# Kernel tuning notes

Measured on AMD Instinct MI355X. Metric: run time of the kernel, lower is better.

Reference implementation:

```python
import jax, jax.numpy as jnp
import numpy as np

N_HEADS = 16
SEG_LEN = 512
MSG_LEN = 1536
T_TOTAL = SEG_LEN + MSG_LEN  # 2048


def _build_mask(T):
    # rows < SEG_LEN: attend to all cols < SEG_LEN (full, non-causal block)
    # rows >= SEG_LEN: standard causal (cols <= row)
    rows = jnp.arange(T)[:, None]
    cols = jnp.arange(T)[None, :]
    mask = jnp.where(rows < SEG_LEN, cols < SEG_LEN, cols <= rows)
    return mask  # [T, T] bool


def setup_inputs() -> dict:
    key = jax.random.key(0)
    k1, k2, k3 = jax.random.split(key, 3)
    B, T, E = 4, T_TOTAL, 1024
    x = jax.random.normal(k1, (B, T, E), dtype=jnp.float32)
    W_qkv = jax.random.normal(k2, (E, 3 * E), dtype=jnp.float32) * (1.0 / np.sqrt(E))
    b_qkv = jnp.zeros((3 * E,), dtype=jnp.float32)
    W_proj = jax.random.normal(k3, (E, E), dtype=jnp.float32) * (1.0 / np.sqrt(E))
    b_proj = jnp.zeros((E,), dtype=jnp.float32)
    return {"x": x, "W_qkv": W_qkv, "b_qkv": b_qkv, "W_proj": W_proj, "b_proj": b_proj}


def reference(x, W_qkv, b_qkv, W_proj, b_proj):
    B, T, E = x.shape
    H = N_HEADS
    D = E // H
    qkv = x @ W_qkv + b_qkv  # [B, T, 3E]
    q, k, v = jnp.split(qkv, 3, axis=-1)
    # [B, H, T, D]
    q = q.reshape(B, T, H, D).transpose(0, 2, 1, 3)
    k = k.reshape(B, T, H, D).transpose(0, 2, 1, 3)
    v = v.reshape(B, T, H, D).transpose(0, 2, 1, 3)
    att = jnp.einsum("bhqd,bhkd->bhqk", q, k) * (1.0 / np.sqrt(D))
    mask = _build_mask(T)  # [T, T]
    att = jnp.where(mask[None, None], att, jnp.float32(-jnp.inf))
    att = jax.nn.softmax(att, axis=-1)
    y = jnp.einsum("bhqk,bhkd->bhqd", att, v)
    y = y.transpose(0, 2, 1, 3).reshape(B, T, E)
    return y @ W_proj + b_proj
```

## Files before the change

### kernel.cpp

```cpp
#include <hip/hip_runtime.h>


typedef _Float16 f16;
typedef _Float16 f16x4 __attribute__((ext_vector_type(4)));
typedef _Float16 f16x8 __attribute__((ext_vector_type(8)));
typedef float f32x4 __attribute__((ext_vector_type(4)));

#define MFMA16x32(a, b, c) __builtin_amdgcn_mfma_f32_16x16x32_f16(a, b, c, 0, 0, 0)
#define MFMA16x16(a, b, c) __builtin_amdgcn_mfma_f32_16x16x16f16(a, b, c, 0, 0, 0)

__device__ __forceinline__ void gload_lds16(const void* g, void* l) {
  __builtin_amdgcn_global_load_lds(
      (__attribute__((address_space(1))) void*)g,
      (__attribute__((address_space(3))) void*)l, 16, 0, 0);
}


__global__ void k_cast_f16(const float* __restrict__ x, f16* __restrict__ xh) {
  int i = blockIdx.x * 256 + threadIdx.x;
  float4 v = ((const float4*)x)[i];
  f16x4 o = {(f16)v.x, (f16)v.y, (f16)v.z, (f16)v.w};
  ((f16x4*)xh)[i] = o;
}

__global__ void k_transpose(const float* __restrict__ W, f16* __restrict__ Wt,
                            int Kdim, int Ndim) {
  __shared__ float tile[32][33];
  int n = blockIdx.x * 32 + threadIdx.x;
  int k0 = blockIdx.y * 32;
  for (int j = threadIdx.y; j < 32; j += 8)
    tile[j][threadIdx.x] = W[(size_t)(k0 + j) * Ndim + n];
  __syncthreads();
  int k = k0 + threadIdx.x;
  for (int j = threadIdx.y; j < 32; j += 8)
    Wt[(size_t)(blockIdx.x * 32 + j) * Kdim + k] = (f16)tile[threadIdx.x][j];
}


__global__ __launch_bounds__(256) void k_gemm_qkv(
    const f16* __restrict__ A, const f16* __restrict__ Bt,
    const float* __restrict__ bias,
    f16* __restrict__ Qo, f16* __restrict__ Ko, f16* __restrict__ Vo) {
  constexpr int KD = 1024;
  __shared__ __align__(16) f16 smem[2 * 128 * 64];
  f16* As = smem;
  f16* Bs = smem + 128 * 64;
  const int tid = threadIdx.x;
  const int wave = tid >> 6, lane = tid & 63;
  const int g = lane >> 4, l16 = lane & 15;
  const int m0 = blockIdx.y * 128, n0 = blockIdx.x * 128;
  const int wm = (wave >> 1) * 64, wn = (wave & 1) * 64;
  const int srow = wave * 8 + (lane >> 3);
  const int skc = ((lane & 7) ^ (lane >> 3)) * 8;

  f32x4 acc[4][4] = {};

  for (int k0 = 0; k0 < KD; k0 += 64) {
    __syncthreads();
    for (int it = 0; it < 4; ++it) {
      gload_lds16(A + (size_t)(m0 + it * 32 + srow) * KD + k0 + skc,
                  As + (it * 32 + wave * 8) * 64);
      gload_lds16(Bt + (size_t)(n0 + it * 32 + srow) * KD + k0 + skc,
                  Bs + (it * 32 + wave * 8) * 64);
    }
    __syncthreads();
    for (int kk = 0; kk < 64; kk += 32) {
      const int ks = kk >> 3;
      f16x8 af[4], bf[4];
      for (int mi = 0; mi < 4; ++mi) {
        int R = wm + mi * 16 + l16, sw = R & 7;
        af[mi] = *(const f16x8*)(As + R * 64 + ((ks + g) ^ sw) * 8);
      }
      for (int ni = 0; ni < 4; ++ni) {
        int R = wn + ni * 16 + l16, sw = R & 7;
        bf[ni] = *(const f16x8*)(Bs + R * 64 + ((ks + g) ^ sw) * 8);
      }
      for (int mi = 0; mi < 4; ++mi)
        for (int ni = 0; ni < 4; ++ni)
          acc[mi][ni] = MFMA16x32(af[mi], bf[ni], acc[mi][ni]);
    }
  }

  const int nsub = n0 + wn;
  const int part = nsub >> 10;
  const int h    = (nsub >> 6) & 15;
  const int mg   = m0 + wm;
  const int b    = mg >> 11;
  const int tb   = mg & 2047;
  const size_t bh = (size_t)(b * 16 + h);

  float bv[4];
  for (int ni = 0; ni < 4; ++ni) bv[ni] = bias[nsub + ni * 16 + l16];

  __syncthreads();
  f16* Es = smem + wave * 4096;

  for (int mi = 0; mi < 4; ++mi)
    for (int ni = 0; ni < 4; ++ni)
      for (int r = 0; r < 4; ++r) {
        f16 hv = (f16)(acc[mi][ni][r] + bv[ni]);
        int mrow = mi * 16 + g * 4 + r, ncol = ni * 16 + l16;
        if (part == 2)
          Es[ncol * 64 + (mrow ^ ((ncol & 7) << 3))] = hv;
        else
          Es[mrow * 64 + (ncol ^ ((mrow & 7) << 3))] = hv;
      }

  const int rrow = lane >> 3, rj = lane & 7;
  for (int p = 0; p < 8; ++p) {
    int row = p * 8 + rrow;
    f16x8 vv = *(const f16x8*)(Es + row * 64 + (rj ^ (row & 7)) * 8);
    int rcol = rj * 8;
    if (part == 0)
      *(f16x8*)(Qo + (bh * 2048 + tb + row) * 64 + rcol) = vv;
    else if (part == 1)
      *(f16x8*)(Ko + (bh * 2048 + tb + row) * 64 + rcol) = vv;
    else
      *(f16x8*)(Vo + (bh * 64 + row) * 2048 + tb + rcol) = vv;
  }
}


__global__ __launch_bounds__(512, 4) void k_attn(
    const f16* __restrict__ Q, const f16* __restrict__ Kb,
    const f16* __restrict__ Vt, f16* __restrict__ Y) {
  __shared__ __align__(16) f16 Ks[2][64 * 64];
  __shared__ __align__(16) f16 Vs[2][64 * 64];
  __shared__ __align__(16) f16 Es[8 * 32 * 72];
  __shared__ float rs[8 * 32];

  const int tid = threadIdx.x;
  const int wave = tid >> 6, lane = tid & 63;
  const int wlo = wave & 3;
  const int g = lane >> 4, l16 = lane & 15;
  const int bh = blockIdx.x;
  const int b = bh >> 4, h = bh & 15;
  const int p = (blockIdx.x + blockIdx.y) & 7;
  const int qa = 15 - 2 * p;
  const int qt = (wave >> 2) ? (qa - 1) : qa;
  const int q0 = qt * 128;
  const int ntq = (qt < 4) ? 8 : (qt + 1) * 2;
  const int nta = (qa < 4) ? 8 : (qa + 1) * 2;
  const int srowrel = lane >> 3;
  const int sc = (lane & 7) ^ srowrel;
  const int srw = wave * 8 + srowrel;

  const f32x4 sinit = {-8.65617025f, -8.65617025f, -8.65617025f, -8.65617025f};

  f16x8 aq[2][2];
  for (int mi = 0; mi < 2; ++mi) {
    const f16* qrow =
        Q + ((size_t)bh * 2048 + q0 + wlo * 32 + mi * 16 + l16) * 64 + g * 8;
    aq[mi][0] = *(const f16x8*)(qrow);
    aq[mi][1] = *(const f16x8*)(qrow + 32);
    for (int kb = 0; kb < 2; ++kb)
      aq[mi][kb] = aq[mi][kb] * (f16)0.18033688f;
  }

  f32x4 o[2][4] = {};
  float rsum[2] = {};

  gload_lds16(Kb + ((size_t)bh * 2048 + srw) * 64 + sc * 8,
              &Ks[0][wave * 8 * 64]);
  gload_lds16(Vt + ((size_t)bh * 64 + srw) * 2048 + sc * 8,
              &Vs[0][wave * 8 * 64]);
  __syncthreads();

  int cur = 0;
  for (int i = 0; i < nta; ++i) {
    if (i + 1 < nta) {
      const int kn0 = (i + 1) << 6;
      gload_lds16(Kb + ((size_t)bh * 2048 + kn0 + srw) * 64 + sc * 8,
                  &Ks[cur ^ 1][wave * 8 * 64]);
      gload_lds16(Vt + ((size_t)bh * 64 + srw) * 2048 + kn0 + sc * 8,
                  &Vs[cur ^ 1][wave * 8 * 64]);
    }

    if (i < ntq) {
      const int kt0 = i << 6;
      const f16* Kc = Ks[cur];
      const f16* Vc = Vs[cur];

      f32x4 t[2][4];
      for (int nb = 0; nb < 4; ++nb) {
        int R = nb * 16 + l16, sw = R & 7;
        f16x8 bk0 = *(const f16x8*)(Kc + R * 64 + ((0 + g) ^ sw) * 8);
        f16x8 bk1 = *(const f16x8*)(Kc + R * 64 + ((4 + g) ^ sw) * 8);
        for (int mi = 0; mi < 2; ++mi) {
          f32x4 acc = MFMA16x32(bk0, aq[mi][0], sinit);
          t[mi][nb] = MFMA16x32(bk1, aq[mi][1], acc);
        }
      }

      const bool masked = (q0 >= 512) && (kt0 >= q0);
      f16x4 ap[4][2];
      for (int mi = 0; mi < 2; ++mi) {
        const int mrow = q0 + wlo * 32 + mi * 16 + l16;
        for (int nb = 0; nb < 4; ++nb)
          for (int r = 0; r < 4; ++r) {
            float pv = __builtin_amdgcn_exp2f(t[mi][nb][r]);
            if (masked && (kt0 + nb * 16 + g * 4 + r > mrow)) pv = 0.f;
            rsum[mi] += pv;
            ap[nb][mi][r] = (f16)pv;
          }
      }

      for (int db = 0; db < 4; ++db)
        for (int nb = 0; nb < 4; ++nb) {
          int R = db * 16 + l16, sw = R & 7;
          int c = nb * 2 + (g >> 1);
          f16x4 bv = *(const f16x4*)(Vc + R * 64 + (c ^ sw) * 8 + (g & 1) * 4);
          for (int mi = 0; mi < 2; ++mi)
            o[mi][db] = MFMA16x16(ap[nb][mi], bv, o[mi][db]);
        }
    }

    __syncthreads();
    cur ^= 1;
  }

  for (int mi = 0; mi < 2; ++mi) {
    rsum[mi] += __shfl_xor(rsum[mi], 16, 64);
    rsum[mi] += __shfl_xor(rsum[mi], 32, 64);
  }

  if (g == 0)
    for (int mi = 0; mi < 2; ++mi) rs[wave * 32 + mi * 16 + l16] = rsum[mi];
  float rinv[2][4];
  for (int mi = 0; mi < 2; ++mi)
    for (int r = 0; r < 4; ++r)
      rinv[mi][r] = 1.0f / rs[wave * 32 + mi * 16 + g * 4 + r];

  f16* Ew = Es + wave * (32 * 72);
  for (int mi = 0; mi < 2; ++mi)
    for (int db = 0; db < 4; ++db)
      for (int r = 0; r < 4; ++r)
        Ew[(mi * 16 + g * 4 + r) * 72 + db * 16 + l16] =
            (f16)(o[mi][db][r] * rinv[mi][r]);

  const int rrow = lane >> 3, rcol = (lane & 7) * 8;
  const size_t ybase = (size_t)b * 2048 + q0 + wlo * 32;
  for (int p2 = 0; p2 < 4; ++p2) {
    int row = p2 * 8 + rrow;
    f16x8 vv = *(const f16x8*)(Ew + row * 72 + rcol);
    *(f16x8*)(Y + (ybase + row) * 1024 + h * 64 + rcol) = vv;
  }
}


__global__ __launch_bounds__(256) void k_gemm_proj(
    const f16* __restrict__ A, const f16* __restrict__ Bt,
    const float* __restrict__ bias, float* __restrict__ out) {
  constexpr int KD = 1024;
  __shared__ __align__(16) f16 As[128 * 64];
  __shared__ __align__(16) f16 Bs[128 * 64];
  const int tid = threadIdx.x;
  const int wave = tid >> 6, lane = tid & 63;
  const int g = lane >> 4, l16 = lane & 15;
  const int m0 = blockIdx.y * 128, n0 = blockIdx.x * 128;
  const int wm = (wave >> 1) * 64, wn = (wave & 1) * 64;
  const int srow = wave * 8 + (lane >> 3);
  const int skc = ((lane & 7) ^ (lane >> 3)) * 8;

  f32x4 acc[4][4] = {};

  for (int k0 = 0; k0 < KD; k0 += 64) {
    __syncthreads();
    for (int it = 0; it < 4; ++it) {
      gload_lds16(A + (size_t)(m0 + it * 32 + srow) * KD + k0 + skc,
                  As + (it * 32 + wave * 8) * 64);
      gload_lds16(Bt + (size_t)(n0 + it * 32 + srow) * KD + k0 + skc,
                  Bs + (it * 32 + wave * 8) * 64);
    }
    __syncthreads();
    for (int kk = 0; kk < 64; kk += 32) {
      const int ks = kk >> 3;
      f16x8 af[4], bf[4];
      for (int mi = 0; mi < 4; ++mi) {
        int R = wm + mi * 16 + l16, sw = R & 7;
        af[mi] = *(const f16x8*)(As + R * 64 + ((ks + g) ^ sw) * 8);
      }
      for (int ni = 0; ni < 4; ++ni) {
        int R = wn + ni * 16 + l16, sw = R & 7;
        bf[ni] = *(const f16x8*)(Bs + R * 64 + ((ks + g) ^ sw) * 8);
      }
      for (int mi = 0; mi < 4; ++mi)
        for (int ni = 0; ni < 4; ++ni)
          acc[mi][ni] = MFMA16x32(af[mi], bf[ni], acc[mi][ni]);
    }
  }

  float bv[4];
  for (int ni = 0; ni < 4; ++ni) bv[ni] = bias[n0 + wn + ni * 16 + l16];

  for (int mi = 0; mi < 4; ++mi)
    for (int ni = 0; ni < 4; ++ni)
      for (int r = 0; r < 4; ++r) {
        int m = m0 + wm + mi * 16 + g * 4 + r;
        int n = n0 + wn + ni * 16 + l16;
        out[(size_t)m * 1024 + n] = acc[mi][ni][r] + bv[ni];
      }
}


extern "C" void kernel_launch(void* const* d_in, const int* in_sizes, int n_in,
                              void* d_out, int out_size, void* d_ws,
                              size_t ws_size, hipStream_t stream) {
  const float* x      = (const float*)d_in[0];
  const float* W_qkv  = (const float*)d_in[1];
  const float* b_qkv  = (const float*)d_in[2];
  const float* W_proj = (const float*)d_in[3];
  const float* b_proj = (const float*)d_in[4];
  float* out = (float*)d_out;

  char* ws = (char*)d_ws;
  f16* xh    = (f16*)ws;   ws += (size_t)8192 * 1024 * 2;
  f16* Wqt   = (f16*)ws;   ws += (size_t)3072 * 1024 * 2;
  f16* Wpt   = (f16*)ws;   ws += (size_t)1024 * 1024 * 2;
  f16* Qb    = (f16*)ws;   ws += (size_t)64 * 2048 * 64 * 2;
  f16* Kb    = (f16*)ws;   ws += (size_t)64 * 2048 * 64 * 2;
  f16* Vt    = (f16*)ws;   ws += (size_t)64 * 64 * 2048 * 2;
  f16* Y = xh;

  k_cast_f16<<<8192, 256, 0, stream>>>(x, xh);
  k_transpose<<<dim3(96, 32), dim3(32, 8), 0, stream>>>(W_qkv, Wqt, 1024, 3072);
  k_transpose<<<dim3(32, 32), dim3(32, 8), 0, stream>>>(W_proj, Wpt, 1024, 1024);
  k_gemm_qkv<<<dim3(24, 64), 256, 0, stream>>>(xh, Wqt, b_qkv, Qb, Kb, Vt);
  k_attn<<<dim3(64, 8), 512, 0, stream>>>(Qb, Kb, Vt, Y);
  k_gemm_proj<<<dim3(8, 64), 256, 0, stream>>>(Y, Wpt, b_proj, out);
}
```

Measured before the change: 287.3 us.

## Merge prep kernels and split attention into one 128-row query tile per block

The cast and two weight transposes are fused into a single launch, so two kernel launches go away. The attention kernel drops its paired-tile scheme: each 512-thread block used to handle two query tiles (long and short) for load balancing, and now each 256-thread block handles one 128-row tile over a 64x16 grid. The output also skips the LDS staging buffer and writes Y with scattered f16 stores. This cuts LDS use and the idle waves in paired blocks, but loses K/V tile sharing across two query tiles and gives the blocks uneven amounts of work.

```diff
diff --git a/kernel.cpp b/kernel.cpp
--- a/kernel.cpp
+++ b/kernel.cpp
@@ -16,24 +16,38 @@
 }
 
 
-__global__ void k_cast_f16(const float* __restrict__ x, f16* __restrict__ xh) {
-  int i = blockIdx.x * 256 + threadIdx.x;
-  float4 v = ((const float4*)x)[i];
-  f16x4 o = {(f16)v.x, (f16)v.y, (f16)v.z, (f16)v.w};
-  ((f16x4*)xh)[i] = o;
-}
-
-__global__ void k_transpose(const float* __restrict__ W, f16* __restrict__ Wt,
-                            int Kdim, int Ndim) {
+__global__ __launch_bounds__(256) void k_prep(
+    const float* __restrict__ x, f16* __restrict__ xh,
+    const float* __restrict__ Wq, f16* __restrict__ Wqt,
+    const float* __restrict__ Wp, f16* __restrict__ Wpt) {
   __shared__ float tile[32][33];
-  int n = blockIdx.x * 32 + threadIdx.x;
-  int k0 = blockIdx.y * 32;
-  for (int j = threadIdx.y; j < 32; j += 8)
-    tile[j][threadIdx.x] = W[(size_t)(k0 + j) * Ndim + n];
+  const int bid = blockIdx.x;
+  if (bid < 8192) {
+    int i = bid * 256 + threadIdx.x;
+    float4 v = ((const float4*)x)[i];
+    f16x4 o = {(f16)v.x, (f16)v.y, (f16)v.z, (f16)v.w};
+    ((f16x4*)xh)[i] = o;
+    return;
+  }
+  const float* W;
+  f16* Wt;
+  int Ndim, bx, by;
+  if (bid < 8192 + 3072) {
+    int r = bid - 8192;
+    W = Wq; Wt = Wqt; Ndim = 3072; bx = r % 96; by = r / 96;
+  } else {
+    int r = bid - 11264;
+    W = Wp; Wt = Wpt; Ndim = 1024; bx = r % 32; by = r / 32;
+  }
+  const int tx = threadIdx.x & 31, ty = threadIdx.x >> 5;
+  const int n = bx * 32 + tx;
+  const int k0 = by * 32;
+  for (int j = ty; j < 32; j += 8)
+    tile[j][tx] = W[(size_t)(k0 + j) * Ndim + n];
   __syncthreads();
-  int k = k0 + threadIdx.x;
-  for (int j = threadIdx.y; j < 32; j += 8)
-    Wt[(size_t)(blockIdx.x * 32 + j) * Kdim + k] = (f16)tile[threadIdx.x][j];
+  const int k = k0 + tx;
+  for (int j = ty; j < 32; j += 8)
+    Wt[(size_t)(bx * 32 + j) * 1024 + k] = (f16)tile[tx][j];
 }
 
 
@@ -121,36 +135,30 @@
 }
 
 
-__global__ __launch_bounds__(512, 4) void k_attn(
+__global__ __launch_bounds__(256, 4) void k_attn(
     const f16* __restrict__ Q, const f16* __restrict__ Kb,
     const f16* __restrict__ Vt, f16* __restrict__ Y) {
   __shared__ __align__(16) f16 Ks[2][64 * 64];
   __shared__ __align__(16) f16 Vs[2][64 * 64];
-  __shared__ __align__(16) f16 Es[8 * 32 * 72];
-  __shared__ float rs[8 * 32];
+  __shared__ float rs[4 * 32];
 
   const int tid = threadIdx.x;
   const int wave = tid >> 6, lane = tid & 63;
-  const int wlo = wave & 3;
   const int g = lane >> 4, l16 = lane & 15;
   const int bh = blockIdx.x;
   const int b = bh >> 4, h = bh & 15;
-  const int p = (blockIdx.x + blockIdx.y) & 7;
-  const int qa = 15 - 2 * p;
-  const int qt = (wave >> 2) ? (qa - 1) : qa;
+  const int qt = 15 - blockIdx.y;
   const int q0 = qt * 128;
-  const int ntq = (qt < 4) ? 8 : (qt + 1) * 2;
-  const int nta = (qa < 4) ? 8 : (qa + 1) * 2;
+  const int nt = (qt < 4) ? 8 : (qt + 1) * 2;
   const int srowrel = lane >> 3;
   const int sc = (lane & 7) ^ srowrel;
-  const int srw = wave * 8 + srowrel;
 
   const f32x4 sinit = {-8.65617025f, -8.65617025f, -8.65617025f, -8.65617025f};
 
   f16x8 aq[2][2];
   for (int mi = 0; mi < 2; ++mi) {
     const f16* qrow =
-        Q + ((size_t)bh * 2048 + q0 + wlo * 32 + mi * 16 + l16) * 64 + g * 8;
+        Q + ((size_t)bh * 2048 + q0 + wave * 32 + mi * 16 + l16) * 64 + g * 8;
     aq[mi][0] = *(const f16x8*)(qrow);
     aq[mi][1] = *(const f16x8*)(qrow + 32);
     for (int kb = 0; kb < 2; ++kb)
@@ -160,60 +168,64 @@
   f32x4 o[2][4] = {};
   float rsum[2] = {};
 
-  gload_lds16(Kb + ((size_t)bh * 2048 + srw) * 64 + sc * 8,
-              &Ks[0][wave * 8 * 64]);
-  gload_lds16(Vt + ((size_t)bh * 64 + srw) * 2048 + sc * 8,
-              &Vs[0][wave * 8 * 64]);
+  for (int it = 0; it < 2; ++it) {
+    int row = it * 32 + wave * 8 + srowrel;
+    gload_lds16(Kb + ((size_t)bh * 2048 + row) * 64 + sc * 8,
+                &Ks[0][(it * 32 + wave * 8) * 64]);
+    gload_lds16(Vt + ((size_t)bh * 64 + row) * 2048 + sc * 8,
+                &Vs[0][(it * 32 + wave * 8) * 64]);
+  }
   __syncthreads();
 
   int cur = 0;
-  for (int i = 0; i < nta; ++i) {
-    if (i + 1 < nta) {
+  for (int i = 0; i < nt; ++i) {
+    if (i + 1 < nt) {
       const int kn0 = (i + 1) << 6;
-      gload_lds16(Kb + ((size_t)bh * 2048 + kn0 + srw) * 64 + sc * 8,
-                  &Ks[cur ^ 1][wave * 8 * 64]);
-      gload_lds16(Vt + ((size_t)bh * 64 + srw) * 2048 + kn0 + sc * 8,
-                  &Vs[cur ^ 1][wave * 8 * 64]);
-    }
-
-    if (i < ntq) {
-      const int kt0 = i << 6;
-      const f16* Kc = Ks[cur];
-      const f16* Vc = Vs[cur];
-
-      f32x4 t[2][4];
+      for (int it = 0; it < 2; ++it) {
+        int row = it * 32 + wave * 8 + srowrel;
+        gload_lds16(Kb + ((size_t)bh * 2048 + kn0 + row) * 64 + sc * 8,
+                    &Ks[cur ^ 1][(it * 32 + wave * 8) * 64]);
+        gload_lds16(Vt + ((size_t)bh * 64 + row) * 2048 + kn0 + sc * 8,
+                    &Vs[cur ^ 1][(it * 32 + wave * 8) * 64]);
+      }
+    }
+
+    const int kt0 = i << 6;
+    const f16* Kc = Ks[cur];
+    const f16* Vc = Vs[cur];
+
+    f32x4 t[2][4];
+    for (int nb = 0; nb < 4; ++nb) {
+      int R = nb * 16 + l16, sw = R & 7;
+      f16x8 bk0 = *(const f16x8*)(Kc + R * 64 + ((0 + g) ^ sw) * 8);
+      f16x8 bk1 = *(const f16x8*)(Kc + R * 64 + ((4 + g) ^ sw) * 8);
+      for (int mi = 0; mi < 2; ++mi) {
+        f32x4 acc = MFMA16x32(bk0, aq[mi][0], sinit);
+        t[mi][nb] = MFMA16x32(bk1, aq[mi][1], acc);
+      }
+    }
+
+    const bool masked = (q0 >= 512) && (kt0 >= q0);
+    f16x4 ap[4][2];
+    for (int mi = 0; mi < 2; ++mi) {
+      const int mrow = q0 + wave * 32 + mi * 16 + l16;
+      for (int nb = 0; nb < 4; ++nb)
+        for (int r = 0; r < 4; ++r) {
+          float pv = __builtin_amdgcn_exp2f(t[mi][nb][r]);
+          if (masked && (kt0 + nb * 16 + g * 4 + r > mrow)) pv = 0.f;
+          rsum[mi] += pv;
+          ap[nb][mi][r] = (f16)pv;
+        }
+    }
+
+    for (int db = 0; db < 4; ++db)
       for (int nb = 0; nb < 4; ++nb) {
-        int R = nb * 16 + l16, sw = R & 7;
-        f16x8 bk0 = *(const f16x8*)(Kc + R * 64 + ((0 + g) ^ sw) * 8);
-        f16x8 bk1 = *(const f16x8*)(Kc + R * 64 + ((4 + g) ^ sw) * 8);
-        for (int mi = 0; mi < 2; ++mi) {
-          f32x4 acc = MFMA16x32(bk0, aq[mi][0], sinit);
-          t[mi][nb] = MFMA16x32(bk1, aq[mi][1], acc);
-        }
-      }
-
-      const bool masked = (q0 >= 512) && (kt0 >= q0);
-      f16x4 ap[4][2];
-      for (int mi = 0; mi < 2; ++mi) {
-        const int mrow = q0 + wlo * 32 + mi * 16 + l16;
-        for (int nb = 0; nb < 4; ++nb)
-          for (int r = 0; r < 4; ++r) {
-            float pv = __builtin_amdgcn_exp2f(t[mi][nb][r]);
-            if (masked && (kt0 + nb * 16 + g * 4 + r > mrow)) pv = 0.f;
-            rsum[mi] += pv;
-            ap[nb][mi][r] = (f16)pv;
-          }
-      }
-
-      for (int db = 0; db < 4; ++db)
-        for (int nb = 0; nb < 4; ++nb) {
-          int R = db * 16 + l16, sw = R & 7;
-          int c = nb * 2 + (g >> 1);
-          f16x4 bv = *(const f16x4*)(Vc + R * 64 + (c ^ sw) * 8 + (g & 1) * 4);
-          for (int mi = 0; mi < 2; ++mi)
-            o[mi][db] = MFMA16x16(ap[nb][mi], bv, o[mi][db]);
-        }
-    }
+        int R = db * 16 + l16, sw = R & 7;
+        int c = nb * 2 + (g >> 1);
+        f16x4 bv = *(const f16x4*)(Vc + R * 64 + (c ^ sw) * 8 + (g & 1) * 4);
+        for (int mi = 0; mi < 2; ++mi)
+          o[mi][db] = MFMA16x16(ap[nb][mi], bv, o[mi][db]);
+      }
 
     __syncthreads();
     cur ^= 1;
@@ -231,20 +243,12 @@
     for (int r = 0; r < 4; ++r)
       rinv[mi][r] = 1.0f / rs[wave * 32 + mi * 16 + g * 4 + r];
 
-  f16* Ew = Es + wave * (32 * 72);
+  const size_t ybase = (size_t)b * 2048 + q0 + wave * 32;
   for (int mi = 0; mi < 2; ++mi)
     for (int db = 0; db < 4; ++db)
       for (int r = 0; r < 4; ++r)
-        Ew[(mi * 16 + g * 4 + r) * 72 + db * 16 + l16] =
+        Y[(ybase + mi * 16 + g * 4 + r) * 1024 + h * 64 + db * 16 + l16] =
             (f16)(o[mi][db][r] * rinv[mi][r]);
-
-  const int rrow = lane >> 3, rcol = (lane & 7) * 8;
-  const size_t ybase = (size_t)b * 2048 + q0 + wlo * 32;
-  for (int p2 = 0; p2 < 4; ++p2) {
-    int row = p2 * 8 + rrow;
-    f16x8 vv = *(const f16x8*)(Ew + row * 72 + rcol);
-    *(f16x8*)(Y + (ybase + row) * 1024 + h * 64 + rcol) = vv;
-  }
 }
 
 
@@ -322,10 +326,8 @@
   f16* Vt    = (f16*)ws;   ws += (size_t)64 * 64 * 2048 * 2;
   f16* Y = xh;
 
-  k_cast_f16<<<8192, 256, 0, stream>>>(x, xh);
-  k_transpose<<<dim3(96, 32), dim3(32, 8), 0, stream>>>(W_qkv, Wqt, 1024, 3072);
-  k_transpose<<<dim3(32, 32), dim3(32, 8), 0, stream>>>(W_proj, Wpt, 1024, 1024);
+  k_prep<<<12288, 256, 0, stream>>>(x, xh, W_qkv, Wqt, W_proj, Wpt);
   k_gemm_qkv<<<dim3(24, 64), 256, 0, stream>>>(xh, Wqt, b_qkv, Qb, Kb, Vt);
-  k_attn<<<dim3(64, 8), 512, 0, stream>>>(Qb, Kb, Vt, Y);
+  k_attn<<<dim3(64, 16), 256, 0, stream>>>(Qb, Kb, Vt, Y);
   k_gemm_proj<<<dim3(8, 64), 256, 0, stream>>>(Y, Wpt, b_proj, out);
 }
```

After: 263.4 us. 1.09x faster.
